# Optimization experiments

Measured on AMD Instinct MI355X. Metric: run time of the kernel, lower is better.

## Reference

```python
import jax, jax.numpy as jnp
import numpy as np

N, E, F_IN, F_E, HID, HEADS = 20000, 320000, 256, 32, 128, 4
NEG_SLOPE = 0.2  # PyG GATConv default negative_slope


def _segment_softmax(logits, seg, num_segments):
    # logits: [E, H] softmax over edges sharing the same destination node
    m = jax.ops.segment_max(logits, seg, num_segments=num_segments)
    m = jnp.where(jnp.isfinite(m), m, 0.0)
    e = jnp.exp(logits - m[seg])
    s = jax.ops.segment_sum(e, seg, num_segments=num_segments)
    return e / s[seg]


def _gat_layer(x, edge_attr, src, dst, W, We, a_src, a_dst, a_edge, bias, num_nodes):
    H, C = a_src.shape
    h = (x @ W).reshape(-1, H, C)            # [N, H, C]
    he = (edge_attr @ We).reshape(-1, H, C)  # [E, H, C]
    alpha = (h * a_src).sum(-1)[src] + (h * a_dst).sum(-1)[dst] + (he * a_edge).sum(-1)
    alpha = jax.nn.leaky_relu(alpha, NEG_SLOPE)          # [E, H]
    alpha = _segment_softmax(alpha, dst, num_nodes)
    out = jax.ops.segment_sum(h[src] * alpha[..., None], dst, num_segments=num_nodes)
    return out.reshape(num_nodes, H * C) + bias


def setup_inputs() -> dict:
    key = jax.random.key(0)
    ks = jax.random.split(key, 20)
    s1 = 1.0 / np.sqrt(F_IN)
    s2 = 1.0 / np.sqrt(HID * HEADS)
    se = 1.0 / np.sqrt(F_E)
    sh = 1.0 / np.sqrt(HID)
    return {
        "x": jax.random.normal(ks[0], (N, F_IN), jnp.float32),
        "edge_index": jax.random.randint(ks[1], (2, E), 0, N),
        "edge_attr": jax.random.normal(ks[2], (E, F_E), jnp.float32),
        # GAT layer 1: in=F_IN, heads=HEADS, out=HID, concat=True
        "W1": jax.random.normal(ks[3], (F_IN, HEADS * HID), jnp.float32) * s1,
        "We1": jax.random.normal(ks[4], (F_E, HEADS * HID), jnp.float32) * se,
        "as1": jax.random.normal(ks[5], (HEADS, HID), jnp.float32) * sh,
        "ad1": jax.random.normal(ks[6], (HEADS, HID), jnp.float32) * sh,
        "ae1": jax.random.normal(ks[7], (HEADS, HID), jnp.float32) * sh,
        "b1": jnp.zeros((HEADS * HID,), jnp.float32),
        # GAT layer 2: in=HEADS*HID, heads=1, out=HID
        "W2": jax.random.normal(ks[8], (HEADS * HID, HID), jnp.float32) * s2,
        "We2": jax.random.normal(ks[9], (F_E, HID), jnp.float32) * se,
        "as2": jax.random.normal(ks[10], (1, HID), jnp.float32) * sh,
        "ad2": jax.random.normal(ks[11], (1, HID), jnp.float32) * sh,
        "ae2": jax.random.normal(ks[12], (1, HID), jnp.float32) * sh,
        "b2": jnp.zeros((HID,), jnp.float32),
        # projection head: Linear(HID,HID) -> PReLU -> Linear(HID,HID)
        "P1": jax.random.normal(ks[13], (HID, HID), jnp.float32) * sh,
        "pb1": jnp.zeros((HID,), jnp.float32),
        "prelu_a": jnp.float32(0.25),
        "P2": jax.random.normal(ks[14], (HID, HID), jnp.float32) * sh,
        "pb2": jnp.zeros((HID,), jnp.float32),
    }


def reference(x, edge_index, edge_attr, W1, We1, as1, ad1, ae1, b1,
              W2, We2, as2, ad2, ae2, b2, P1, pb1, prelu_a, P2, pb2):
    # eval mode: edge dropout / feature dropout are no-ops
    ei = jnp.concatenate([edge_index, edge_index[::-1]], axis=1)  # add reversed edges
    ea = jnp.concatenate([edge_attr, edge_attr], axis=0)
    src, dst = ei[0], ei[1]
    n = x.shape[0]
    h = jax.nn.elu(_gat_layer(x, ea, src, dst, W1, We1, as1, ad1, ae1, b1, n))
    h = jax.nn.elu(_gat_layer(h, ea, src, dst, W2, We2, as2, ad2, ae2, b2, n))
    z = h @ P1 + pb1
    z = jnp.where(z > 0, z, prelu_a * z)  # PReLU (single shared parameter)
    h_proj = z @ P2 + pb2
    g = jax.nn.sigmoid(h_proj.mean(axis=0))
    return h_proj, g
```

## Files before the change

### kernel.cpp

```cpp
#include <hip/hip_runtime.h>
#include <hip/hip_bf16.h>


#define NN    20000
#define EE    320000
#define E2    640000
#define FIN   256
#define FE    32
#define HIDD  128
#define NHEAD 4
#define HH    512

typedef unsigned short ushort_t;
typedef short frag8 __attribute__((ext_vector_type(8)));
typedef float f32x4 __attribute__((ext_vector_type(4)));

__device__ inline ushort_t f2bf(float f){
  unsigned x = __float_as_uint(f);
  unsigned r = (x + 0x7fffu + ((x>>16)&1u)) >> 16;
  return (ushort_t)r;
}
__device__ inline float bf2f(ushort_t u){ return __uint_as_float(((unsigned)u)<<16); }
__device__ inline float lo_of(unsigned v){ return __uint_as_float(v<<16); }
__device__ inline float hi_of(unsigned v){ return __uint_as_float(v & 0xffff0000u); }

__global__ void prep(const int* __restrict__ ei, int* __restrict__ cnt,
                     const float* __restrict__ x, ushort_t* __restrict__ xb,
                     const float* __restrict__ W1, ushort_t* __restrict__ W1t,
                     const float* __restrict__ W2, ushort_t* __restrict__ W2t,
                     const float* __restrict__ P1, ushort_t* __restrict__ P1th, ushort_t* __restrict__ P1tl,
                     const float* __restrict__ P2, ushort_t* __restrict__ P2th, ushort_t* __restrict__ P2tl,
                     const float* __restrict__ We1, const float* __restrict__ ae1,
                     const float* __restrict__ We2, const float* __restrict__ ae2,
                     float* __restrict__ v1, float* __restrict__ v2){
  int b = blockIdx.x, tid = threadIdx.x;
  if(b < 2500){
    int e = b*256 + tid;
    int dst = (e < EE) ? ei[EE + e] : ei[e - EE];
    atomicAdd(&cnt[dst], 1);
  } else if(b < 7500){
    int i = (b-2500)*256 + tid;
    float4 v = ((const float4*)x)[i];
    ushort4 o; o.x=f2bf(v.x); o.y=f2bf(v.y); o.z=f2bf(v.z); o.w=f2bf(v.w);
    ((ushort4*)xb)[i] = o;
  } else if(b < 8012){
    int idx = (b-7500)*256 + tid;
    int k = idx>>9, n = idx&511;
    W1t[n*FIN + k] = f2bf(W1[idx]);
  } else if(b < 8268){
    int idx = (b-8012)*256 + tid;
    int k = idx>>7, n = idx&127;
    W2t[n*HH + k] = f2bf(W2[idx]);
  } else if(b < 8332){
    int idx = (b-8268)*256 + tid;
    int k = idx>>7, n = idx&127;
    float v = P1[idx];
    ushort_t h = f2bf(v);
    P1th[n*HIDD + k] = h;
    P1tl[n*HIDD + k] = f2bf(v - bf2f(h));
  } else if(b < 8396){
    int idx = (b-8332)*256 + tid;
    int k = idx>>7, n = idx&127;
    float v = P2[idx];
    ushort_t h = f2bf(v);
    P2th[n*HIDD + k] = h;
    P2tl[n*HIDD + k] = f2bf(v - bf2f(h));
  } else {
    if(tid < FE*NHEAD){
      int f = tid>>2, h = tid&3;
      float s = 0.f;
      for(int c=0;c<HIDD;c++) s += We1[f*HH + h*HIDD + c] * ae1[h*HIDD + c];
      v1[f*4+h] = s;
    } else if(tid < FE*NHEAD + FE){
      int f = tid - FE*NHEAD;
      float s = 0.f;
      for(int c=0;c<HIDD;c++) s += We2[f*HIDD + c] * ae2[c];
      v2[f] = s;
    }
  }
}

__global__ void scan_k(const int* __restrict__ cnt, int* __restrict__ rowptr){
  __shared__ int sums[1024];
  int tid = threadIdx.x;
  const int per = (NN + 1023)/1024;
  int base = tid*per;
  int s = 0;
  for(int i=0;i<per;i++){ int idx=base+i; if(idx<NN) s += cnt[idx]; }
  sums[tid] = s; __syncthreads();
  for(int off=1; off<1024; off<<=1){
    int v = (tid>=off)? sums[tid-off] : 0;
    __syncthreads();
    sums[tid] += v;
    __syncthreads();
  }
  int run = (tid==0)? 0 : sums[tid-1];
  for(int i=0;i<per;i++){
    int idx = base+i;
    if(idx<=NN) rowptr[idx] = run;
    if(idx<NN)  run += cnt[idx];
  }
}

__global__ void csr_fill(const int* __restrict__ ei, const float* __restrict__ ea,
                         const float* __restrict__ v1, const float* __restrict__ v2,
                         const int* __restrict__ rowptr, int* __restrict__ fcnt,
                         int* __restrict__ csrc, float* __restrict__ cae1, float* __restrict__ cae2){
  __shared__ float sv1[FE*NHEAD];
  __shared__ float sv2[FE];
  int tid = threadIdx.x;
  if(tid < FE*NHEAD) sv1[tid] = v1[tid];
  if(tid < FE)       sv2[tid] = v2[tid];
  __syncthreads();
  int e = blockIdx.x*256 + tid;
  int a = ei[e], b = ei[EE+e];
  const float4* er4 = (const float4*)(ea + (long)e*FE);
  float a0=0,a1=0,a2=0,a3=0,ab=0;
  #pragma unroll
  for(int f4=0; f4<FE/4; f4++){
    float4 t = er4[f4];
    float tv[4] = {t.x, t.y, t.z, t.w};
    #pragma unroll
    for(int c=0;c<4;c++){
      int f = f4*4+c;
      float t1 = tv[c];
      a0 += t1*sv1[f*4+0]; a1 += t1*sv1[f*4+1]; a2 += t1*sv1[f*4+2]; a3 += t1*sv1[f*4+3];
      ab += t1*sv2[f];
    }
  }
  float4 c4; c4.x=a0; c4.y=a1; c4.z=a2; c4.w=a3;
  int pos = rowptr[b] + atomicAdd(&fcnt[b], 1);
  csrc[pos] = a;
  *(float4*)(cae1 + (size_t)pos*4) = c4;
  cae2[pos] = ab;
  pos = rowptr[a] + atomicAdd(&fcnt[a], 1);
  csrc[pos] = b;
  *(float4*)(cae1 + (size_t)pos*4) = c4;
  cae2[pos] = ab;
}

__global__ __launch_bounds__(256) void gemm1_attn(const ushort_t* __restrict__ A, const ushort_t* __restrict__ Bt,
                                                  ushort_t* __restrict__ C, int M,
                                                  const float* __restrict__ as1, const float* __restrict__ ad1,
                                                  float* __restrict__ s1n, float* __restrict__ d1n){
  __shared__ ushort_t As[128*32];
  __shared__ ushort_t Bs[128*32];
  __shared__ float sred[2][128], dred[2][128];
  int tid = threadIdx.x;
  int head = blockIdx.x;
  int m0 = blockIdx.y*128, n0 = head*128;
  int w = tid>>6, lane = tid&63;
  int qr = (w>>1)*64, qc = (w&1)*64;
  int lrow = lane&15, koff = (lane>>4)*8;
  f32x4 acc[4][4] = {};
  for(int k0=0; k0<FIN; k0+=32){
    #pragma unroll
    for(int rep=0;rep<2;rep++){
      int segid = tid + rep*256;
      int row = segid>>2, off = (segid&3)*8;
      int gr = m0 + row;
      int4 va = (gr<M) ? *(const int4*)(A + (long)gr*FIN + k0 + off) : int4{0,0,0,0};
      *(int4*)&As[row*32 + off] = va;
      int4 vb = *(const int4*)(Bt + (long)(n0+row)*FIN + k0 + off);
      *(int4*)&Bs[row*32 + off] = vb;
    }
    __syncthreads();
    frag8 af[4], bfr[4];
    #pragma unroll
    for(int i=0;i<4;i++) af[i]  = *(const frag8*)&As[(qr + i*16 + lrow)*32 + koff];
    #pragma unroll
    for(int j=0;j<4;j++) bfr[j] = *(const frag8*)&Bs[(qc + j*16 + lrow)*32 + koff];
    #pragma unroll
    for(int i=0;i<4;i++)
      #pragma unroll
      for(int j=0;j<4;j++)
        acc[i][j] = __builtin_amdgcn_mfma_f32_16x16x32_bf16(af[i], bfr[j], acc[i][j], 0,0,0);
    __syncthreads();
  }
  #pragma unroll
  for(int i=0;i<4;i++)
    #pragma unroll
    for(int j=0;j<4;j++)
      #pragma unroll
      for(int r=0;r<4;r++){
        int row = m0 + qr + i*16 + (lane>>4)*4 + r;
        int col = n0 + qc + j*16 + (lane&15);
        if(row<M) C[(long)row*HH + col] = f2bf(acc[i][j][r]);
      }
  float a_s[4], a_d[4];
  #pragma unroll
  for(int j=0;j<4;j++){
    a_s[j] = as1[head*HIDD + qc + j*16 + (lane&15)];
    a_d[j] = ad1[head*HIDD + qc + j*16 + (lane&15)];
  }
  #pragma unroll
  for(int i=0;i<4;i++)
    #pragma unroll
    for(int r=0;r<4;r++){
      float sp = acc[i][0][r]*a_s[0] + acc[i][1][r]*a_s[1] + acc[i][2][r]*a_s[2] + acc[i][3][r]*a_s[3];
      float dp = acc[i][0][r]*a_d[0] + acc[i][1][r]*a_d[1] + acc[i][2][r]*a_d[2] + acc[i][3][r]*a_d[3];
      #pragma unroll
      for(int o=1;o<=8;o<<=1){ sp += __shfl_xor(sp,o,64); dp += __shfl_xor(dp,o,64); }
      if((lane&15)==0){
        int rl = qr + i*16 + (lane>>4)*4 + r;
        sred[w&1][rl] = sp;
        dred[w&1][rl] = dp;
      }
    }
  __syncthreads();
  if(tid < 128){
    int gr = m0 + tid;
    if(gr < M){
      s1n[gr*4 + head] = sred[0][tid] + sred[1][tid];
      d1n[gr*4 + head] = dred[0][tid] + dred[1][tid];
    }
  }
}

__global__ __launch_bounds__(256) void gemm64_attn(const ushort_t* __restrict__ A, const ushort_t* __restrict__ Bt,
                                                   ushort_t* __restrict__ C, int M,
                                                   const float* __restrict__ as2, const float* __restrict__ ad2,
                                                   float* __restrict__ s2n, float* __restrict__ d2n){
  __shared__ ushort_t As[64*32];
  __shared__ ushort_t Bs[128*32];
  __shared__ float sred[4][64], dred[4][64];
  int tid = threadIdx.x;
  int m0 = blockIdx.y*64;
  int w = tid>>6, lane = tid&63;
  int qc = w*32;
  int lrow = lane&15, koff = (lane>>4)*8;
  f32x4 acc[4][2] = {};
  for(int k0=0; k0<HH; k0+=32){
    {
      int row = tid>>2, off = (tid&3)*8;
      int gr = m0 + row;
      int4 va = (gr<M) ? *(const int4*)(A + (long)gr*HH + k0 + off) : int4{0,0,0,0};
      *(int4*)&As[row*32 + off] = va;
    }
    #pragma unroll
    for(int rep=0;rep<2;rep++){
      int segid = tid + rep*256;
      int row = segid>>2, off = (segid&3)*8;
      int4 vb = *(const int4*)(Bt + (long)row*HH + k0 + off);
      *(int4*)&Bs[row*32 + off] = vb;
    }
    __syncthreads();
    frag8 af[4], bfr[2];
    #pragma unroll
    for(int i=0;i<4;i++) af[i]  = *(const frag8*)&As[(i*16 + lrow)*32 + koff];
    #pragma unroll
    for(int j=0;j<2;j++) bfr[j] = *(const frag8*)&Bs[(qc + j*16 + lrow)*32 + koff];
    #pragma unroll
    for(int i=0;i<4;i++)
      #pragma unroll
      for(int j=0;j<2;j++)
        acc[i][j] = __builtin_amdgcn_mfma_f32_16x16x32_bf16(af[i], bfr[j], acc[i][j], 0,0,0);
    __syncthreads();
  }
  #pragma unroll
  for(int i=0;i<4;i++)
    #pragma unroll
    for(int j=0;j<2;j++)
      #pragma unroll
      for(int r=0;r<4;r++){
        int row = m0 + i*16 + (lane>>4)*4 + r;
        int col = qc + j*16 + (lane&15);
        if(row<M) C[(long)row*HIDD + col] = f2bf(acc[i][j][r]);
      }
  float a_s[2], a_d[2];
  #pragma unroll
  for(int j=0;j<2;j++){
    a_s[j] = as2[qc + j*16 + (lane&15)];
    a_d[j] = ad2[qc + j*16 + (lane&15)];
  }
  #pragma unroll
  for(int i=0;i<4;i++)
    #pragma unroll
    for(int r=0;r<4;r++){
      float sp = acc[i][0][r]*a_s[0] + acc[i][1][r]*a_s[1];
      float dp = acc[i][0][r]*a_d[0] + acc[i][1][r]*a_d[1];
      #pragma unroll
      for(int o=1;o<=8;o<<=1){ sp += __shfl_xor(sp,o,64); dp += __shfl_xor(dp,o,64); }
      if((lane&15)==0){
        int rl = i*16 + (lane>>4)*4 + r;
        sred[w][rl] = sp;
        dred[w][rl] = dp;
      }
    }
  __syncthreads();
  if(tid < 64){
    int gr = m0 + tid;
    if(gr < M){
      s2n[gr] = sred[0][tid]+sred[1][tid]+sred[2][tid]+sred[3][tid];
      d2n[gr] = dred[0][tid]+dred[1][tid]+dred[2][tid]+dred[3][tid];
    }
  }
}

__global__ __launch_bounds__(256) void mfma_proj(const float* __restrict__ A,
                                                 const ushort_t* __restrict__ Bth, const ushort_t* __restrict__ Btl,
                                                 float* __restrict__ C, int M,
                                                 const float* __restrict__ bias,
                                                 const float* __restrict__ prelu_a, int epi,
                                                 float* __restrict__ gbuf){
  __shared__ ushort_t Ash[64*32], Asl[64*32];
  __shared__ ushort_t Bsh[128*32], Bsl[128*32];
  int tid = threadIdx.x;
  int m0 = blockIdx.x*64;
  int w = tid>>6, lane = tid&63;
  int qc = w*32;
  int lrow = lane&15, koff2 = (lane>>4)*8;
  f32x4 acc[4][2] = {};
  for(int k0=0; k0<128; k0+=32){
    {
      int row = tid>>2, koff = (tid&3)*8;
      int gr = m0 + row;
      float4 u0{0,0,0,0}, u1{0,0,0,0};
      if(gr<M){
        u0 = *(const float4*)(A + (long)gr*HIDD + k0 + koff);
        u1 = *(const float4*)(A + (long)gr*HIDD + k0 + koff + 4);
      }
      float vv[8] = {u0.x,u0.y,u0.z,u0.w,u1.x,u1.y,u1.z,u1.w};
      unsigned ph[4], pl[4];
      #pragma unroll
      for(int c=0;c<4;c++){
        ushort_t h0 = f2bf(vv[2*c]),   l0 = f2bf(vv[2*c]   - bf2f(h0));
        ushort_t h1 = f2bf(vv[2*c+1]), l1 = f2bf(vv[2*c+1] - bf2f(h1));
        ph[c] = (unsigned)h0 | ((unsigned)h1<<16);
        pl[c] = (unsigned)l0 | ((unsigned)l1<<16);
      }
      *(uint4*)&Ash[row*32 + koff] = *(uint4*)ph;
      *(uint4*)&Asl[row*32 + koff] = *(uint4*)pl;
    }
    #pragma unroll
    for(int rep=0;rep<2;rep++){
      int segid = tid + rep*256;
      int row = segid>>2, off = (segid&3)*8;
      *(int4*)&Bsh[row*32 + off] = *(const int4*)(Bth + (long)row*HIDD + k0 + off);
      *(int4*)&Bsl[row*32 + off] = *(const int4*)(Btl + (long)row*HIDD + k0 + off);
    }
    __syncthreads();
    frag8 afh[4], afl[4], bfh[2], bfl[2];
    #pragma unroll
    for(int i=0;i<4;i++){
      afh[i] = *(const frag8*)&Ash[(i*16 + lrow)*32 + koff2];
      afl[i] = *(const frag8*)&Asl[(i*16 + lrow)*32 + koff2];
    }
    #pragma unroll
    for(int j=0;j<2;j++){
      bfh[j] = *(const frag8*)&Bsh[(qc + j*16 + lrow)*32 + koff2];
      bfl[j] = *(const frag8*)&Bsl[(qc + j*16 + lrow)*32 + koff2];
    }
    #pragma unroll
    for(int i=0;i<4;i++)
      #pragma unroll
      for(int j=0;j<2;j++){
        acc[i][j] = __builtin_amdgcn_mfma_f32_16x16x32_bf16(afh[i], bfh[j], acc[i][j], 0,0,0);
        acc[i][j] = __builtin_amdgcn_mfma_f32_16x16x32_bf16(afh[i], bfl[j], acc[i][j], 0,0,0);
        acc[i][j] = __builtin_amdgcn_mfma_f32_16x16x32_bf16(afl[i], bfh[j], acc[i][j], 0,0,0);
      }
    __syncthreads();
  }
  float ap = (epi==1)? prelu_a[0] : 0.f;
  #pragma unroll
  for(int i=0;i<4;i++)
    #pragma unroll
    for(int j=0;j<2;j++)
      #pragma unroll
      for(int r=0;r<4;r++){
        int row = m0 + i*16 + (lane>>4)*4 + r;
        int col = qc + j*16 + (lane&15);
        if(row<M){
          float v = acc[i][j][r] + bias[col];
          if(epi==1) v = v>0.f? v : ap*v;
          acc[i][j][r] = v;
          C[(long)row*HIDD + col] = v;
        } else acc[i][j][r] = 0.f;
      }
  if(epi==0){
    #pragma unroll
    for(int j=0;j<2;j++){
      float cp = 0.f;
      #pragma unroll
      for(int i=0;i<4;i++)
        #pragma unroll
        for(int r=0;r<4;r++) cp += acc[i][j][r];
      cp += __shfl_xor(cp,16,64);
      cp += __shfl_xor(cp,32,64);
      if((lane>>4)==0) atomicAdd(&gbuf[qc + j*16 + (lane&15)], cp);
    }
  }
}


__global__ __launch_bounds__(512) void agg1(const ushort_t* __restrict__ h1b, const int* __restrict__ rowptr,
                     const int* __restrict__ csrc,
                     const float* __restrict__ s1n, const float* __restrict__ d1n,
                     const float* __restrict__ cae1, float* __restrict__ elog,
                     const float* __restrict__ b1, ushort_t* __restrict__ out1b){
  __shared__ float part[4][512];
  int tid = threadIdx.x;
  int nodeLoc = tid>>7;
  int wv = (tid>>6)&1;
  int lane = tid&63;
  int n = blockIdx.x*4 + nodeLoc;
  int beg = rowptr[n], end = rowptr[n+1];
  int h12 = lane&3;
  float dh = d1n[n*4 + h12];
  float m = -1e30f, ss = 0.f;
  for(int base=beg; base<end; base+=16){
    int e = base + (lane>>2);
    if(e<end){
      float t = s1n[csrc[e]*4 + h12] + dh + cae1[e*4 + h12];
      t = t>0.f? t : 0.2f*t;
      if(wv==0) elog[e*4 + h12] = t;
      float nm = fmaxf(m, t);
      ss = ss*__expf(m-nm) + __expf(t-nm);
      m = nm;
    }
  }
  #pragma unroll
  for(int o=4;o<=32;o<<=1){
    float mo = __shfl_xor(m, o, 64), so = __shfl_xor(ss, o, 64);
    float nm = fmaxf(m, mo);
    ss = ss*__expf(m-nm) + so*__expf(mo-nm);
    m = nm;
  }
  float inv = ss>0.f ? 1.f/ss : 0.f;
  int hq = lane>>4;
  float mq   = __shfl(m,   hq, 64);
  float invq = __shfl(inv, hq, 64);
  __syncthreads();
  int deg = end-beg;
  int half = (deg+1)>>1;
  int gb = beg + wv*half;
  int ge = wv ? end : beg+half;
  float acc[8] = {};
  int i = gb;
  for(; i+3<ge; i+=4){
    int s0 = csrc[i], s1 = csrc[i+1], s2 = csrc[i+2], s3 = csrc[i+3];
    float w0 = __expf(elog[i*4 + hq]     - mq)*invq;
    float w1 = __expf(elog[(i+1)*4 + hq] - mq)*invq;
    float w2 = __expf(elog[(i+2)*4 + hq] - mq)*invq;
    float w3 = __expf(elog[(i+3)*4 + hq] - mq)*invq;
    uint4 v0 = *(const uint4*)(h1b + (long)s0*HH + lane*8);
    uint4 v1 = *(const uint4*)(h1b + (long)s1*HH + lane*8);
    uint4 v2 = *(const uint4*)(h1b + (long)s2*HH + lane*8);
    uint4 v3 = *(const uint4*)(h1b + (long)s3*HH + lane*8);
    acc[0] += w0*lo_of(v0.x) + w1*lo_of(v1.x) + w2*lo_of(v2.x) + w3*lo_of(v3.x);
    acc[1] += w0*hi_of(v0.x) + w1*hi_of(v1.x) + w2*hi_of(v2.x) + w3*hi_of(v3.x);
    acc[2] += w0*lo_of(v0.y) + w1*lo_of(v1.y) + w2*lo_of(v2.y) + w3*lo_of(v3.y);
    acc[3] += w0*hi_of(v0.y) + w1*hi_of(v1.y) + w2*hi_of(v2.y) + w3*hi_of(v3.y);
    acc[4] += w0*lo_of(v0.z) + w1*lo_of(v1.z) + w2*lo_of(v2.z) + w3*lo_of(v3.z);
    acc[5] += w0*hi_of(v0.z) + w1*hi_of(v1.z) + w2*hi_of(v2.z) + w3*hi_of(v3.z);
    acc[6] += w0*lo_of(v0.w) + w1*lo_of(v1.w) + w2*lo_of(v2.w) + w3*lo_of(v3.w);
    acc[7] += w0*hi_of(v0.w) + w1*hi_of(v1.w) + w2*hi_of(v2.w) + w3*hi_of(v3.w);
  }
  for(; i<ge; i++){
    int s0 = csrc[i];
    float w0 = __expf(elog[i*4 + hq] - mq)*invq;
    uint4 v0 = *(const uint4*)(h1b + (long)s0*HH + lane*8);
    acc[0] += w0*lo_of(v0.x); acc[1] += w0*hi_of(v0.x);
    acc[2] += w0*lo_of(v0.y); acc[3] += w0*hi_of(v0.y);
    acc[4] += w0*lo_of(v0.z); acc[5] += w0*hi_of(v0.z);
    acc[6] += w0*lo_of(v0.w); acc[7] += w0*hi_of(v0.w);
  }
  if(wv==1){
    #pragma unroll
    for(int c=0;c<8;c++) part[nodeLoc][c*64 + lane] = acc[c];
  }
  __syncthreads();
  if(wv==0){
    #pragma unroll
    for(int c=0;c<8;c++) acc[c] += part[nodeLoc][c*64 + lane];
    float4 bl = ((const float4*)b1)[lane*2];
    float4 bh = ((const float4*)b1)[lane*2+1];
    float bb[8] = {bl.x,bl.y,bl.z,bl.w,bh.x,bh.y,bh.z,bh.w};
    ushort_t o8[8];
    #pragma unroll
    for(int c=0;c<8;c++){
      float o = acc[c] + bb[c];
      o8[c] = f2bf(o>0.f? o : __expf(o)-1.f);
    }
    uint4 pk;
    pk.x = (unsigned)o8[0] | ((unsigned)o8[1]<<16);
    pk.y = (unsigned)o8[2] | ((unsigned)o8[3]<<16);
    pk.z = (unsigned)o8[4] | ((unsigned)o8[5]<<16);
    pk.w = (unsigned)o8[6] | ((unsigned)o8[7]<<16);
    *(uint4*)(out1b + (long)n*HH + lane*8) = pk;
  }
}

__global__ void agg2(const ushort_t* __restrict__ h2b, const int* __restrict__ rowptr,
                     const int* __restrict__ csrc,
                     const float* __restrict__ s2n, const float* __restrict__ d2n,
                     const float* __restrict__ cae2, float* __restrict__ elog,
                     const float* __restrict__ b2, float* __restrict__ out2){
  int n = blockIdx.x*4 + (threadIdx.x>>6);
  int lane = threadIdx.x&63;
  int beg = rowptr[n], end = rowptr[n+1];
  float dn = d2n[n];
  float m = -1e30f, ss = 0.f;
  for(int e=beg+lane; e<end; e+=64){
    float t = s2n[csrc[e]] + dn + cae2[e];
    t = t>0.f? t : 0.2f*t;
    elog[e] = t;
    float nm = fmaxf(m, t);
    ss = ss*__expf(m-nm) + __expf(t-nm);
    m = nm;
  }
  #pragma unroll
  for(int o=1;o<=32;o<<=1){
    float mo = __shfl_xor(m, o, 64), so = __shfl_xor(ss, o, 64);
    float nm = fmaxf(m, mo);
    ss = ss*__expf(m-nm) + so*__expf(mo-nm);
    m = nm;
  }
  float inv = ss>0.f ? 1.f/ss : 0.f;
  float a0=0.f, a1=0.f;
  int i = beg;
  for(; i+3<end; i+=4){
    int s0 = csrc[i], s1 = csrc[i+1], s2 = csrc[i+2], s3 = csrc[i+3];
    float w0 = __expf(elog[i]-m)*inv;
    float w1 = __expf(elog[i+1]-m)*inv;
    float w2 = __expf(elog[i+2]-m)*inv;
    float w3 = __expf(elog[i+3]-m)*inv;
    unsigned v0 = *(const unsigned*)(h2b + (long)s0*HIDD + 2*lane);
    unsigned v1 = *(const unsigned*)(h2b + (long)s1*HIDD + 2*lane);
    unsigned v2 = *(const unsigned*)(h2b + (long)s2*HIDD + 2*lane);
    unsigned v3 = *(const unsigned*)(h2b + (long)s3*HIDD + 2*lane);
    a0 += w0*lo_of(v0) + w1*lo_of(v1) + w2*lo_of(v2) + w3*lo_of(v3);
    a1 += w0*hi_of(v0) + w1*hi_of(v1) + w2*hi_of(v2) + w3*hi_of(v3);
  }
  for(; i<end; i++){
    float w0 = __expf(elog[i]-m)*inv;
    unsigned v0 = *(const unsigned*)(h2b + (long)csrc[i]*HIDD + 2*lane);
    a0 += w0*lo_of(v0); a1 += w0*hi_of(v0);
  }
  float o0 = a0 + b2[2*lane];
  float o1 = a1 + b2[2*lane+1];
  float2 pk;
  pk.x = o0>0.f? o0 : __expf(o0)-1.f;
  pk.y = o1>0.f? o1 : __expf(o1)-1.f;
  *(float2*)(out2 + (long)n*HIDD + 2*lane) = pk;
}

__global__ void sigmoid_g(const float* __restrict__ gbuf, float* __restrict__ gout){
  int c = threadIdx.x;
  float m = gbuf[c] * (1.0f/NN);
  gout[c] = 1.f/(1.f+__expf(-m));
}


extern "C" void kernel_launch(void* const* d_in, const int* in_sizes, int n_in,
                              void* d_out, int out_size, void* d_ws, size_t ws_size,
                              hipStream_t stream){
  const float* x    = (const float*)d_in[0];
  const int*   ei   = (const int*)  d_in[1];
  const float* ea   = (const float*)d_in[2];
  const float* W1   = (const float*)d_in[3];
  const float* We1  = (const float*)d_in[4];
  const float* as1  = (const float*)d_in[5];
  const float* ad1  = (const float*)d_in[6];
  const float* ae1  = (const float*)d_in[7];
  const float* b1   = (const float*)d_in[8];
  const float* W2   = (const float*)d_in[9];
  const float* We2  = (const float*)d_in[10];
  const float* as2  = (const float*)d_in[11];
  const float* ad2  = (const float*)d_in[12];
  const float* ae2  = (const float*)d_in[13];
  const float* b2   = (const float*)d_in[14];
  const float* P1   = (const float*)d_in[15];
  const float* pb1  = (const float*)d_in[16];
  const float* pra  = (const float*)d_in[17];
  const float* P2   = (const float*)d_in[18];
  const float* pb2  = (const float*)d_in[19];
  float* out = (float*)d_out;

  char* wsp = (char*)d_ws;
  size_t off = 0;
  auto alloc = [&](size_t bytes)->char*{
    char* p = wsp + off;
    off += (bytes + 255) & ~(size_t)255;
    return p;
  };
  ushort_t* h1b  = (ushort_t*)alloc(sizeof(ushort_t)*(size_t)NN*HH);
  ushort_t* out1b= (ushort_t*)alloc(sizeof(ushort_t)*(size_t)NN*HH);
  ushort_t* h2b  = (ushort_t*)alloc(sizeof(ushort_t)*(size_t)NN*HIDD);
  float*    out2 = (float*)  alloc(sizeof(float)*(size_t)NN*HIDD);
  float*    zb   = (float*)  alloc(sizeof(float)*(size_t)NN*HIDD);
  ushort_t* xb   = (ushort_t*)alloc(sizeof(ushort_t)*(size_t)NN*FIN);
  ushort_t* W1t  = (ushort_t*)alloc(sizeof(ushort_t)*(size_t)HH*FIN);
  ushort_t* W2t  = (ushort_t*)alloc(sizeof(ushort_t)*(size_t)HIDD*HH);
  ushort_t* P1th = (ushort_t*)alloc(sizeof(ushort_t)*(size_t)HIDD*HIDD);
  ushort_t* P1tl = (ushort_t*)alloc(sizeof(ushort_t)*(size_t)HIDD*HIDD);
  ushort_t* P2th = (ushort_t*)alloc(sizeof(ushort_t)*(size_t)HIDD*HIDD);
  ushort_t* P2tl = (ushort_t*)alloc(sizeof(ushort_t)*(size_t)HIDD*HIDD);
  float* s1n   = (float*)alloc(sizeof(float)*NN*NHEAD);
  float* d1n   = (float*)alloc(sizeof(float)*NN*NHEAD);
  float* s2n   = (float*)alloc(sizeof(float)*NN);
  float* d2n   = (float*)alloc(sizeof(float)*NN);
  float* v1    = (float*)alloc(sizeof(float)*FE*NHEAD);
  float* v2    = (float*)alloc(sizeof(float)*FE);
  float* cae1  = (float*)alloc(sizeof(float)*(size_t)E2*NHEAD);
  float* elog1 = (float*)alloc(sizeof(float)*(size_t)E2*NHEAD);
  float* cae2  = (float*)alloc(sizeof(float)*(size_t)E2);
  float* elog2 = (float*)alloc(sizeof(float)*(size_t)E2);
  int*   rowptr= (int*)  alloc(sizeof(int)*(NN+1));
  int*   csrc  = (int*)  alloc(sizeof(int)*(size_t)E2);
  int*   cnt   = (int*)  alloc(sizeof(int)*NN);
  int*   fcnt  = (int*)  alloc(sizeof(int)*NN);
  float* gbuf  = (float*)alloc(sizeof(float)*HIDD);

  hipMemsetAsync(cnt, 0, 80128 + 80128 + 512, stream);

  prep    <<<8397, 256, 0, stream>>>(ei, cnt, x, xb, W1, W1t, W2, W2t,
                                     P1, P1th, P1tl, P2, P2th, P2tl,
                                     We1, ae1, We2, ae2, v1, v2);
  scan_k  <<<1, 1024, 0, stream>>>(cnt, rowptr);
  csr_fill<<<EE/256, 256, 0, stream>>>(ei, ea, v1, v2, rowptr, fcnt, csrc, cae1, cae2);

  gemm1_attn<<<dim3(NHEAD, (NN+127)/128), 256, 0, stream>>>(xb, W1t, h1b, NN, as1, ad1, s1n, d1n);
  agg1      <<<NN/4, 512, 0, stream>>>(h1b, rowptr, csrc, s1n, d1n, cae1, elog1, b1, out1b);

  gemm64_attn<<<dim3(1, (NN+63)/64), 256, 0, stream>>>(out1b, W2t, h2b, NN, as2, ad2, s2n, d2n);
  agg2       <<<NN/4, 256, 0, stream>>>(h2b, rowptr, csrc, s2n, d2n, cae2, elog2, b2, out2);

  mfma_proj<<<(NN+63)/64, 256, 0, stream>>>(out2, P1th, P1tl, zb, NN, pb1, pra, 1, nullptr);
  mfma_proj<<<(NN+63)/64, 256, 0, stream>>>(zb,  P2th, P2tl, out, NN, pb2, nullptr, 0, gbuf);

  sigmoid_g<<<1, 128, 0, stream>>>(gbuf, out + (size_t)NN*HIDD);
}
```

Baseline: 432.7 us.

## Fuse CSR fill with GEMM1, cache logits in LDS, fuse projection GEMMs

The CSR fill and the first attention GEMM now run in one launch, with the first 1250 blocks doing edge work and the rest doing GEMM tiles, so the two independent stages can overlap. Both aggregation kernels keep per-edge logits and source indices in LDS (up to CAP edges per node) and no longer write or read global elog buffers. agg1 now uses one wave per node instead of two waves splitting each node's edges. The two projection GEMMs are merged into one kernel that keeps the PReLU intermediate in LDS, which drops the zb round trip through global memory. The costs are larger LDS footprint, a recompute path for nodes above CAP, and less parallelism per node in agg1.

```diff
diff --git a/kernel.cpp b/kernel.cpp
--- a/kernel.cpp
+++ b/kernel.cpp
@@ -10,6 +10,8 @@
 #define HIDD  128
 #define NHEAD 4
 #define HH    512
+#define CAP   160
+#define AW    132
 
 typedef unsigned short ushort_t;
 typedef short frag8 __attribute__((ext_vector_type(8)));
@@ -102,53 +104,56 @@
   }
 }
 
-__global__ void csr_fill(const int* __restrict__ ei, const float* __restrict__ ea,
-                         const float* __restrict__ v1, const float* __restrict__ v2,
-                         const int* __restrict__ rowptr, int* __restrict__ fcnt,
-                         int* __restrict__ csrc, float* __restrict__ cae1, float* __restrict__ cae2){
+__global__ __launch_bounds__(256) void csr_gemm1(
+    const int* __restrict__ ei, const float* __restrict__ ea,
+    const float* __restrict__ v1, const float* __restrict__ v2,
+    const int* __restrict__ rowptr, int* __restrict__ fcnt,
+    int* __restrict__ csrc, float* __restrict__ cae1, float* __restrict__ cae2,
+    const ushort_t* __restrict__ A, const ushort_t* __restrict__ Bt,
+    ushort_t* __restrict__ C, int M,
+    const float* __restrict__ as1, const float* __restrict__ ad1,
+    float* __restrict__ s1n, float* __restrict__ d1n){
+  __shared__ ushort_t As[128*32];
+  __shared__ ushort_t Bs[128*32];
+  __shared__ float sred[2][128], dred[2][128];
   __shared__ float sv1[FE*NHEAD];
   __shared__ float sv2[FE];
   int tid = threadIdx.x;
-  if(tid < FE*NHEAD) sv1[tid] = v1[tid];
-  if(tid < FE)       sv2[tid] = v2[tid];
-  __syncthreads();
-  int e = blockIdx.x*256 + tid;
-  int a = ei[e], b = ei[EE+e];
-  const float4* er4 = (const float4*)(ea + (long)e*FE);
-  float a0=0,a1=0,a2=0,a3=0,ab=0;
-  #pragma unroll
-  for(int f4=0; f4<FE/4; f4++){
-    float4 t = er4[f4];
-    float tv[4] = {t.x, t.y, t.z, t.w};
-    #pragma unroll
-    for(int c=0;c<4;c++){
-      int f = f4*4+c;
-      float t1 = tv[c];
-      a0 += t1*sv1[f*4+0]; a1 += t1*sv1[f*4+1]; a2 += t1*sv1[f*4+2]; a3 += t1*sv1[f*4+3];
-      ab += t1*sv2[f];
-    }
-  }
-  float4 c4; c4.x=a0; c4.y=a1; c4.z=a2; c4.w=a3;
-  int pos = rowptr[b] + atomicAdd(&fcnt[b], 1);
-  csrc[pos] = a;
-  *(float4*)(cae1 + (size_t)pos*4) = c4;
-  cae2[pos] = ab;
-  pos = rowptr[a] + atomicAdd(&fcnt[a], 1);
-  csrc[pos] = b;
-  *(float4*)(cae1 + (size_t)pos*4) = c4;
-  cae2[pos] = ab;
-}
-
-__global__ __launch_bounds__(256) void gemm1_attn(const ushort_t* __restrict__ A, const ushort_t* __restrict__ Bt,
-                                                  ushort_t* __restrict__ C, int M,
-                                                  const float* __restrict__ as1, const float* __restrict__ ad1,
-                                                  float* __restrict__ s1n, float* __restrict__ d1n){
-  __shared__ ushort_t As[128*32];
-  __shared__ ushort_t Bs[128*32];
-  __shared__ float sred[2][128], dred[2][128];
-  int tid = threadIdx.x;
-  int head = blockIdx.x;
-  int m0 = blockIdx.y*128, n0 = head*128;
+  int b = blockIdx.x;
+  if(b < 1250){
+    if(tid < FE*NHEAD) sv1[tid] = v1[tid];
+    if(tid < FE)       sv2[tid] = v2[tid];
+    __syncthreads();
+    int e = b*256 + tid;
+    int a = ei[e], bb = ei[EE+e];
+    const float4* er4 = (const float4*)(ea + (long)e*FE);
+    float a0=0,a1=0,a2=0,a3=0,ab=0;
+    #pragma unroll
+    for(int f4=0; f4<FE/4; f4++){
+      float4 t = er4[f4];
+      float tv[4] = {t.x, t.y, t.z, t.w};
+      #pragma unroll
+      for(int c=0;c<4;c++){
+        int f = f4*4+c;
+        float t1 = tv[c];
+        a0 += t1*sv1[f*4+0]; a1 += t1*sv1[f*4+1]; a2 += t1*sv1[f*4+2]; a3 += t1*sv1[f*4+3];
+        ab += t1*sv2[f];
+      }
+    }
+    float4 c4; c4.x=a0; c4.y=a1; c4.z=a2; c4.w=a3;
+    int pos = rowptr[bb] + atomicAdd(&fcnt[bb], 1);
+    csrc[pos] = a;
+    *(float4*)(cae1 + (size_t)pos*4) = c4;
+    cae2[pos] = ab;
+    pos = rowptr[a] + atomicAdd(&fcnt[a], 1);
+    csrc[pos] = bb;
+    *(float4*)(cae1 + (size_t)pos*4) = c4;
+    cae2[pos] = ab;
+    return;
+  }
+  int g = b - 1250;
+  int head = g & 3;
+  int m0 = (g>>2)*128, n0 = head*128;
   int w = tid>>6, lane = tid&63;
   int qr = (w>>1)*64, qc = (w&1)*64;
   int lrow = lane&15, koff = (lane>>4)*8;
@@ -297,123 +302,32 @@
   }
 }
 
-__global__ __launch_bounds__(256) void mfma_proj(const float* __restrict__ A,
-                                                 const ushort_t* __restrict__ Bth, const ushort_t* __restrict__ Btl,
-                                                 float* __restrict__ C, int M,
-                                                 const float* __restrict__ bias,
-                                                 const float* __restrict__ prelu_a, int epi,
-                                                 float* __restrict__ gbuf){
-  __shared__ ushort_t Ash[64*32], Asl[64*32];
-  __shared__ ushort_t Bsh[128*32], Bsl[128*32];
-  int tid = threadIdx.x;
-  int m0 = blockIdx.x*64;
-  int w = tid>>6, lane = tid&63;
-  int qc = w*32;
-  int lrow = lane&15, koff2 = (lane>>4)*8;
-  f32x4 acc[4][2] = {};
-  for(int k0=0; k0<128; k0+=32){
-    {
-      int row = tid>>2, koff = (tid&3)*8;
-      int gr = m0 + row;
-      float4 u0{0,0,0,0}, u1{0,0,0,0};
-      if(gr<M){
-        u0 = *(const float4*)(A + (long)gr*HIDD + k0 + koff);
-        u1 = *(const float4*)(A + (long)gr*HIDD + k0 + koff + 4);
-      }
-      float vv[8] = {u0.x,u0.y,u0.z,u0.w,u1.x,u1.y,u1.z,u1.w};
-      unsigned ph[4], pl[4];
-      #pragma unroll
-      for(int c=0;c<4;c++){
-        ushort_t h0 = f2bf(vv[2*c]),   l0 = f2bf(vv[2*c]   - bf2f(h0));
-        ushort_t h1 = f2bf(vv[2*c+1]), l1 = f2bf(vv[2*c+1] - bf2f(h1));
-        ph[c] = (unsigned)h0 | ((unsigned)h1<<16);
-        pl[c] = (unsigned)l0 | ((unsigned)l1<<16);
-      }
-      *(uint4*)&Ash[row*32 + koff] = *(uint4*)ph;
-      *(uint4*)&Asl[row*32 + koff] = *(uint4*)pl;
-    }
-    #pragma unroll
-    for(int rep=0;rep<2;rep++){
-      int segid = tid + rep*256;
-      int row = segid>>2, off = (segid&3)*8;
-      *(int4*)&Bsh[row*32 + off] = *(const int4*)(Bth + (long)row*HIDD + k0 + off);
-      *(int4*)&Bsl[row*32 + off] = *(const int4*)(Btl + (long)row*HIDD + k0 + off);
-    }
-    __syncthreads();
-    frag8 afh[4], afl[4], bfh[2], bfl[2];
-    #pragma unroll
-    for(int i=0;i<4;i++){
-      afh[i] = *(const frag8*)&Ash[(i*16 + lrow)*32 + koff2];
-      afl[i] = *(const frag8*)&Asl[(i*16 + lrow)*32 + koff2];
-    }
-    #pragma unroll
-    for(int j=0;j<2;j++){
-      bfh[j] = *(const frag8*)&Bsh[(qc + j*16 + lrow)*32 + koff2];
-      bfl[j] = *(const frag8*)&Bsl[(qc + j*16 + lrow)*32 + koff2];
-    }
-    #pragma unroll
-    for(int i=0;i<4;i++)
-      #pragma unroll
-      for(int j=0;j<2;j++){
-        acc[i][j] = __builtin_amdgcn_mfma_f32_16x16x32_bf16(afh[i], bfh[j], acc[i][j], 0,0,0);
-        acc[i][j] = __builtin_amdgcn_mfma_f32_16x16x32_bf16(afh[i], bfl[j], acc[i][j], 0,0,0);
-        acc[i][j] = __builtin_amdgcn_mfma_f32_16x16x32_bf16(afl[i], bfh[j], acc[i][j], 0,0,0);
-      }
-    __syncthreads();
-  }
-  float ap = (epi==1)? prelu_a[0] : 0.f;
-  #pragma unroll
-  for(int i=0;i<4;i++)
-    #pragma unroll
-    for(int j=0;j<2;j++)
-      #pragma unroll
-      for(int r=0;r<4;r++){
-        int row = m0 + i*16 + (lane>>4)*4 + r;
-        int col = qc + j*16 + (lane&15);
-        if(row<M){
-          float v = acc[i][j][r] + bias[col];
-          if(epi==1) v = v>0.f? v : ap*v;
-          acc[i][j][r] = v;
-          C[(long)row*HIDD + col] = v;
-        } else acc[i][j][r] = 0.f;
-      }
-  if(epi==0){
-    #pragma unroll
-    for(int j=0;j<2;j++){
-      float cp = 0.f;
-      #pragma unroll
-      for(int i=0;i<4;i++)
-        #pragma unroll
-        for(int r=0;r<4;r++) cp += acc[i][j][r];
-      cp += __shfl_xor(cp,16,64);
-      cp += __shfl_xor(cp,32,64);
-      if((lane>>4)==0) atomicAdd(&gbuf[qc + j*16 + (lane&15)], cp);
-    }
-  }
-}
-
-
-__global__ __launch_bounds__(512) void agg1(const ushort_t* __restrict__ h1b, const int* __restrict__ rowptr,
+__global__ __launch_bounds__(256) void agg1(const ushort_t* __restrict__ h1b, const int* __restrict__ rowptr,
                      const int* __restrict__ csrc,
                      const float* __restrict__ s1n, const float* __restrict__ d1n,
-                     const float* __restrict__ cae1, float* __restrict__ elog,
+                     const float* __restrict__ cae1,
                      const float* __restrict__ b1, ushort_t* __restrict__ out1b){
-  __shared__ float part[4][512];
+  __shared__ float stlog[4][CAP*4];
+  __shared__ int   sidx[4][CAP];
   int tid = threadIdx.x;
-  int nodeLoc = tid>>7;
-  int wv = (tid>>6)&1;
-  int lane = tid&63;
-  int n = blockIdx.x*4 + nodeLoc;
+  int wv = tid>>6, lane = tid&63;
+  int n = blockIdx.x*4 + wv;
   int beg = rowptr[n], end = rowptr[n+1];
+  int deg = end - beg;
   int h12 = lane&3;
   float dh = d1n[n*4 + h12];
   float m = -1e30f, ss = 0.f;
   for(int base=beg; base<end; base+=16){
     int e = base + (lane>>2);
     if(e<end){
-      float t = s1n[csrc[e]*4 + h12] + dh + cae1[e*4 + h12];
+      int s = csrc[e];
+      float t = s1n[s*4 + h12] + dh + cae1[e*4 + h12];
       t = t>0.f? t : 0.2f*t;
-      if(wv==0) elog[e*4 + h12] = t;
+      int j = e - beg;
+      if(j < CAP){
+        stlog[wv][j*4 + h12] = t;
+        if(h12==0) sidx[wv][j] = s;
+      }
       float nm = fmaxf(m, t);
       ss = ss*__expf(m-nm) + __expf(t-nm);
       m = nm;
@@ -430,19 +344,16 @@
   int hq = lane>>4;
   float mq   = __shfl(m,   hq, 64);
   float invq = __shfl(inv, hq, 64);
-  __syncthreads();
-  int deg = end-beg;
-  int half = (deg+1)>>1;
-  int gb = beg + wv*half;
-  int ge = wv ? end : beg+half;
+  float dhq  = d1n[n*4 + hq];
+  int capn = deg < CAP ? deg : CAP;
   float acc[8] = {};
-  int i = gb;
-  for(; i+3<ge; i+=4){
-    int s0 = csrc[i], s1 = csrc[i+1], s2 = csrc[i+2], s3 = csrc[i+3];
-    float w0 = __expf(elog[i*4 + hq]     - mq)*invq;
-    float w1 = __expf(elog[(i+1)*4 + hq] - mq)*invq;
-    float w2 = __expf(elog[(i+2)*4 + hq] - mq)*invq;
-    float w3 = __expf(elog[(i+3)*4 + hq] - mq)*invq;
+  int j = 0;
+  for(; j+3<capn; j+=4){
+    int s0 = sidx[wv][j], s1 = sidx[wv][j+1], s2 = sidx[wv][j+2], s3 = sidx[wv][j+3];
+    float w0 = __expf(stlog[wv][(j  )*4 + hq] - mq)*invq;
+    float w1 = __expf(stlog[wv][(j+1)*4 + hq] - mq)*invq;
+    float w2 = __expf(stlog[wv][(j+2)*4 + hq] - mq)*invq;
+    float w3 = __expf(stlog[wv][(j+3)*4 + hq] - mq)*invq;
     uint4 v0 = *(const uint4*)(h1b + (long)s0*HH + lane*8);
     uint4 v1 = *(const uint4*)(h1b + (long)s1*HH + lane*8);
     uint4 v2 = *(const uint4*)(h1b + (long)s2*HH + lane*8);
@@ -456,55 +367,64 @@
     acc[6] += w0*lo_of(v0.w) + w1*lo_of(v1.w) + w2*lo_of(v2.w) + w3*lo_of(v3.w);
     acc[7] += w0*hi_of(v0.w) + w1*hi_of(v1.w) + w2*hi_of(v2.w) + w3*hi_of(v3.w);
   }
-  for(; i<ge; i++){
-    int s0 = csrc[i];
-    float w0 = __expf(elog[i*4 + hq] - mq)*invq;
+  for(; j<capn; j++){
+    int s0 = sidx[wv][j];
+    float w0 = __expf(stlog[wv][j*4 + hq] - mq)*invq;
     uint4 v0 = *(const uint4*)(h1b + (long)s0*HH + lane*8);
     acc[0] += w0*lo_of(v0.x); acc[1] += w0*hi_of(v0.x);
     acc[2] += w0*lo_of(v0.y); acc[3] += w0*hi_of(v0.y);
     acc[4] += w0*lo_of(v0.z); acc[5] += w0*hi_of(v0.z);
     acc[6] += w0*lo_of(v0.w); acc[7] += w0*hi_of(v0.w);
   }
-  if(wv==1){
-    #pragma unroll
-    for(int c=0;c<8;c++) part[nodeLoc][c*64 + lane] = acc[c];
-  }
-  __syncthreads();
-  if(wv==0){
-    #pragma unroll
-    for(int c=0;c<8;c++) acc[c] += part[nodeLoc][c*64 + lane];
-    float4 bl = ((const float4*)b1)[lane*2];
-    float4 bh = ((const float4*)b1)[lane*2+1];
-    float bb[8] = {bl.x,bl.y,bl.z,bl.w,bh.x,bh.y,bh.z,bh.w};
-    ushort_t o8[8];
-    #pragma unroll
-    for(int c=0;c<8;c++){
-      float o = acc[c] + bb[c];
-      o8[c] = f2bf(o>0.f? o : __expf(o)-1.f);
-    }
-    uint4 pk;
-    pk.x = (unsigned)o8[0] | ((unsigned)o8[1]<<16);
-    pk.y = (unsigned)o8[2] | ((unsigned)o8[3]<<16);
-    pk.z = (unsigned)o8[4] | ((unsigned)o8[5]<<16);
-    pk.w = (unsigned)o8[6] | ((unsigned)o8[7]<<16);
-    *(uint4*)(out1b + (long)n*HH + lane*8) = pk;
-  }
-}
-
-__global__ void agg2(const ushort_t* __restrict__ h2b, const int* __restrict__ rowptr,
+  for(; j<deg; j++){
+    int e = beg + j;
+    int s0 = csrc[e];
+    float t = s1n[s0*4 + hq] + dhq + cae1[e*4 + hq];
+    t = t>0.f? t : 0.2f*t;
+    float w0 = __expf(t - mq)*invq;
+    uint4 v0 = *(const uint4*)(h1b + (long)s0*HH + lane*8);
+    acc[0] += w0*lo_of(v0.x); acc[1] += w0*hi_of(v0.x);
+    acc[2] += w0*lo_of(v0.y); acc[3] += w0*hi_of(v0.y);
+    acc[4] += w0*lo_of(v0.z); acc[5] += w0*hi_of(v0.z);
+    acc[6] += w0*lo_of(v0.w); acc[7] += w0*hi_of(v0.w);
+  }
+  float4 bl = ((const float4*)b1)[lane*2];
+  float4 bh = ((const float4*)b1)[lane*2+1];
+  float bb[8] = {bl.x,bl.y,bl.z,bl.w,bh.x,bh.y,bh.z,bh.w};
+  ushort_t o8[8];
+  #pragma unroll
+  for(int c=0;c<8;c++){
+    float o = acc[c] + bb[c];
+    o8[c] = f2bf(o>0.f? o : __expf(o)-1.f);
+  }
+  uint4 pk;
+  pk.x = (unsigned)o8[0] | ((unsigned)o8[1]<<16);
+  pk.y = (unsigned)o8[2] | ((unsigned)o8[3]<<16);
+  pk.z = (unsigned)o8[4] | ((unsigned)o8[5]<<16);
+  pk.w = (unsigned)o8[6] | ((unsigned)o8[7]<<16);
+  *(uint4*)(out1b + (long)n*HH + lane*8) = pk;
+}
+
+__global__ __launch_bounds__(256) void agg2(const ushort_t* __restrict__ h2b, const int* __restrict__ rowptr,
                      const int* __restrict__ csrc,
                      const float* __restrict__ s2n, const float* __restrict__ d2n,
-                     const float* __restrict__ cae2, float* __restrict__ elog,
+                     const float* __restrict__ cae2,
                      const float* __restrict__ b2, float* __restrict__ out2){
-  int n = blockIdx.x*4 + (threadIdx.x>>6);
-  int lane = threadIdx.x&63;
+  __shared__ float stl[4][CAP];
+  __shared__ int   sid[4][CAP];
+  int tid = threadIdx.x;
+  int wv = tid>>6, lane = tid&63;
+  int n = blockIdx.x*4 + wv;
   int beg = rowptr[n], end = rowptr[n+1];
+  int deg = end - beg;
   float dn = d2n[n];
   float m = -1e30f, ss = 0.f;
   for(int e=beg+lane; e<end; e+=64){
-    float t = s2n[csrc[e]] + dn + cae2[e];
+    int s = csrc[e];
+    float t = s2n[s] + dn + cae2[e];
     t = t>0.f? t : 0.2f*t;
-    elog[e] = t;
+    int j = e - beg;
+    if(j < CAP){ stl[wv][j] = t; sid[wv][j] = s; }
     float nm = fmaxf(m, t);
     ss = ss*__expf(m-nm) + __expf(t-nm);
     m = nm;
@@ -517,14 +437,15 @@
     m = nm;
   }
   float inv = ss>0.f ? 1.f/ss : 0.f;
+  int capn = deg < CAP ? deg : CAP;
   float a0=0.f, a1=0.f;
-  int i = beg;
-  for(; i+3<end; i+=4){
-    int s0 = csrc[i], s1 = csrc[i+1], s2 = csrc[i+2], s3 = csrc[i+3];
-    float w0 = __expf(elog[i]-m)*inv;
-    float w1 = __expf(elog[i+1]-m)*inv;
-    float w2 = __expf(elog[i+2]-m)*inv;
-    float w3 = __expf(elog[i+3]-m)*inv;
+  int j = 0;
+  for(; j+3<capn; j+=4){
+    int s0 = sid[wv][j], s1 = sid[wv][j+1], s2 = sid[wv][j+2], s3 = sid[wv][j+3];
+    float w0 = __expf(stl[wv][j]  -m)*inv;
+    float w1 = __expf(stl[wv][j+1]-m)*inv;
+    float w2 = __expf(stl[wv][j+2]-m)*inv;
+    float w3 = __expf(stl[wv][j+3]-m)*inv;
     unsigned v0 = *(const unsigned*)(h2b + (long)s0*HIDD + 2*lane);
     unsigned v1 = *(const unsigned*)(h2b + (long)s1*HIDD + 2*lane);
     unsigned v2 = *(const unsigned*)(h2b + (long)s2*HIDD + 2*lane);
@@ -532,9 +453,18 @@
     a0 += w0*lo_of(v0) + w1*lo_of(v1) + w2*lo_of(v2) + w3*lo_of(v3);
     a1 += w0*hi_of(v0) + w1*hi_of(v1) + w2*hi_of(v2) + w3*hi_of(v3);
   }
-  for(; i<end; i++){
-    float w0 = __expf(elog[i]-m)*inv;
-    unsigned v0 = *(const unsigned*)(h2b + (long)csrc[i]*HIDD + 2*lane);
+  for(; j<capn; j++){
+    float w0 = __expf(stl[wv][j]-m)*inv;
+    unsigned v0 = *(const unsigned*)(h2b + (long)sid[wv][j]*HIDD + 2*lane);
+    a0 += w0*lo_of(v0); a1 += w0*hi_of(v0);
+  }
+  for(; j<deg; j++){
+    int e = beg + j;
+    int s0 = csrc[e];
+    float t = s2n[s0] + dn + cae2[e];
+    t = t>0.f? t : 0.2f*t;
+    float w0 = __expf(t-m)*inv;
+    unsigned v0 = *(const unsigned*)(h2b + (long)s0*HIDD + 2*lane);
     a0 += w0*lo_of(v0); a1 += w0*hi_of(v0);
   }
   float o0 = a0 + b2[2*lane];
@@ -543,6 +473,143 @@
   pk.x = o0>0.f? o0 : __expf(o0)-1.f;
   pk.y = o1>0.f? o1 : __expf(o1)-1.f;
   *(float2*)(out2 + (long)n*HIDD + 2*lane) = pk;
+}
+
+__global__ __launch_bounds__(256) void proj_fused(const float* __restrict__ A,
+    const ushort_t* __restrict__ P1th, const ushort_t* __restrict__ P1tl,
+    const ushort_t* __restrict__ P2th, const ushort_t* __restrict__ P2tl,
+    const float* __restrict__ pb1, const float* __restrict__ pra,
+    const float* __restrict__ pb2, float* __restrict__ OUT, int M,
+    float* __restrict__ gbuf){
+  __shared__ ushort_t Ah[64*AW], Al[64*AW];
+  __shared__ ushort_t Bh[128*32], Bl[128*32];
+  int tid = threadIdx.x;
+  int m0 = blockIdx.x*64;
+  int w = tid>>6, lane = tid&63;
+  int qc = w*32;
+  int lrow = lane&15, koff2 = (lane>>4)*8;
+  f32x4 acc[4][2] = {};
+  {
+    int row = tid>>2, cb = (tid&3)*8;
+    int gr = m0 + row;
+    for(int c0=0;c0<HIDD;c0+=32){
+      float4 u0{0,0,0,0}, u1{0,0,0,0};
+      if(gr<M){
+        u0 = *(const float4*)(A + (long)gr*HIDD + c0 + cb);
+        u1 = *(const float4*)(A + (long)gr*HIDD + c0 + cb + 4);
+      }
+      float vv[8] = {u0.x,u0.y,u0.z,u0.w,u1.x,u1.y,u1.z,u1.w};
+      unsigned ph[4], pl[4];
+      #pragma unroll
+      for(int c=0;c<4;c++){
+        ushort_t h0 = f2bf(vv[2*c]),   l0 = f2bf(vv[2*c]   - bf2f(h0));
+        ushort_t h1 = f2bf(vv[2*c+1]), l1 = f2bf(vv[2*c+1] - bf2f(h1));
+        ph[c] = (unsigned)h0 | ((unsigned)h1<<16);
+        pl[c] = (unsigned)l0 | ((unsigned)l1<<16);
+      }
+      *(uint4*)&Ah[row*AW + c0 + cb] = *(uint4*)ph;
+      *(uint4*)&Al[row*AW + c0 + cb] = *(uint4*)pl;
+    }
+  }
+  __syncthreads();
+  for(int k0=0;k0<HIDD;k0+=32){
+    #pragma unroll
+    for(int rep=0;rep<2;rep++){
+      int segid = tid + rep*256;
+      int row = segid>>2, off = (segid&3)*8;
+      *(int4*)&Bh[row*32 + off] = *(const int4*)(P1th + (long)row*HIDD + k0 + off);
+      *(int4*)&Bl[row*32 + off] = *(const int4*)(P1tl + (long)row*HIDD + k0 + off);
+    }
+    __syncthreads();
+    frag8 afh[4], afl[4], bfh[2], bfl[2];
+    #pragma unroll
+    for(int i=0;i<4;i++){
+      afh[i] = *(const frag8*)&Ah[(i*16 + lrow)*AW + k0 + koff2];
+      afl[i] = *(const frag8*)&Al[(i*16 + lrow)*AW + k0 + koff2];
+    }
+    #pragma unroll
+    for(int j=0;j<2;j++){
+      bfh[j] = *(const frag8*)&Bh[(qc + j*16 + lrow)*32 + koff2];
+      bfl[j] = *(const frag8*)&Bl[(qc + j*16 + lrow)*32 + koff2];
+    }
+    #pragma unroll
+    for(int i=0;i<4;i++)
+      #pragma unroll
+      for(int j=0;j<2;j++){
+        acc[i][j] = __builtin_amdgcn_mfma_f32_16x16x32_bf16(afh[i], bfh[j], acc[i][j], 0,0,0);
+        acc[i][j] = __builtin_amdgcn_mfma_f32_16x16x32_bf16(afh[i], bfl[j], acc[i][j], 0,0,0);
+        acc[i][j] = __builtin_amdgcn_mfma_f32_16x16x32_bf16(afl[i], bfh[j], acc[i][j], 0,0,0);
+      }
+    __syncthreads();
+  }
+  float ap = pra[0];
+  #pragma unroll
+  for(int i=0;i<4;i++)
+    #pragma unroll
+    for(int j=0;j<2;j++)
+      #pragma unroll
+      for(int r=0;r<4;r++){
+        int row = i*16 + (lane>>4)*4 + r;
+        int col = qc + j*16 + (lane&15);
+        float v = acc[i][j][r] + pb1[col];
+        v = v>0.f? v : ap*v;
+        ushort_t h = f2bf(v);
+        Ah[row*AW + col] = h;
+        Al[row*AW + col] = f2bf(v - bf2f(h));
+        acc[i][j][r] = 0.f;
+      }
+  __syncthreads();
+  for(int k0=0;k0<HIDD;k0+=32){
+    #pragma unroll
+    for(int rep=0;rep<2;rep++){
+      int segid = tid + rep*256;
+      int row = segid>>2, off = (segid&3)*8;
+      *(int4*)&Bh[row*32 + off] = *(const int4*)(P2th + (long)row*HIDD + k0 + off);
+      *(int4*)&Bl[row*32 + off] = *(const int4*)(P2tl + (long)row*HIDD + k0 + off);
+    }
+    __syncthreads();
+    frag8 afh[4], afl[4], bfh[2], bfl[2];
+    #pragma unroll
+    for(int i=0;i<4;i++){
+      afh[i] = *(const frag8*)&Ah[(i*16 + lrow)*AW + k0 + koff2];
+      afl[i] = *(const frag8*)&Al[(i*16 + lrow)*AW + k0 + koff2];
+    }
+    #pragma unroll
+    for(int j=0;j<2;j++){
+      bfh[j] = *(const frag8*)&Bh[(qc + j*16 + lrow)*32 + koff2];
+      bfl[j] = *(const frag8*)&Bl[(qc + j*16 + lrow)*32 + koff2];
+    }
+    #pragma unroll
+    for(int i=0;i<4;i++)
+      #pragma unroll
+      for(int j=0;j<2;j++){
+        acc[i][j] = __builtin_amdgcn_mfma_f32_16x16x32_bf16(afh[i], bfh[j], acc[i][j], 0,0,0);
+        acc[i][j] = __builtin_amdgcn_mfma_f32_16x16x32_bf16(afh[i], bfl[j], acc[i][j], 0,0,0);
+        acc[i][j] = __builtin_amdgcn_mfma_f32_16x16x32_bf16(afl[i], bfh[j], acc[i][j], 0,0,0);
+      }
+    __syncthreads();
+  }
+  float cs[2] = {0.f, 0.f};
+  #pragma unroll
+  for(int i=0;i<4;i++)
+    #pragma unroll
+    for(int j=0;j<2;j++)
+      #pragma unroll
+      for(int r=0;r<4;r++){
+        int rowg = m0 + i*16 + (lane>>4)*4 + r;
+        int col = qc + j*16 + (lane&15);
+        if(rowg<M){
+          float v = acc[i][j][r] + pb2[col];
+          OUT[(long)rowg*HIDD + col] = v;
+          cs[j] += v;
+        }
+      }
+  #pragma unroll
+  for(int j=0;j<2;j++){
+    cs[j] += __shfl_xor(cs[j],16,64);
+    cs[j] += __shfl_xor(cs[j],32,64);
+    if((lane>>4)==0) atomicAdd(&gbuf[qc + j*16 + (lane&15)], cs[j]);
+  }
 }
 
 __global__ void sigmoid_g(const float* __restrict__ gbuf, float* __restrict__ gout){
@@ -588,7 +655,6 @@
   ushort_t* out1b= (ushort_t*)alloc(sizeof(ushort_t)*(size_t)NN*HH);
   ushort_t* h2b  = (ushort_t*)alloc(sizeof(ushort_t)*(size_t)NN*HIDD);
   float*    out2 = (float*)  alloc(sizeof(float)*(size_t)NN*HIDD);
-  float*    zb   = (float*)  alloc(sizeof(float)*(size_t)NN*HIDD);
   ushort_t* xb   = (ushort_t*)alloc(sizeof(ushort_t)*(size_t)NN*FIN);
   ushort_t* W1t  = (ushort_t*)alloc(sizeof(ushort_t)*(size_t)HH*FIN);
   ushort_t* W2t  = (ushort_t*)alloc(sizeof(ushort_t)*(size_t)HIDD*HH);
@@ -603,9 +669,7 @@
   float* v1    = (float*)alloc(sizeof(float)*FE*NHEAD);
   float* v2    = (float*)alloc(sizeof(float)*FE);
   float* cae1  = (float*)alloc(sizeof(float)*(size_t)E2*NHEAD);
-  float* elog1 = (float*)alloc(sizeof(float)*(size_t)E2*NHEAD);
   float* cae2  = (float*)alloc(sizeof(float)*(size_t)E2);
-  float* elog2 = (float*)alloc(sizeof(float)*(size_t)E2);
   int*   rowptr= (int*)  alloc(sizeof(int)*(NN+1));
   int*   csrc  = (int*)  alloc(sizeof(int)*(size_t)E2);
   int*   cnt   = (int*)  alloc(sizeof(int)*NN);
@@ -614,20 +678,16 @@
 
   hipMemsetAsync(cnt, 0, 80128 + 80128 + 512, stream);
 
-  prep    <<<8397, 256, 0, stream>>>(ei, cnt, x, xb, W1, W1t, W2, W2t,
-                                     P1, P1th, P1tl, P2, P2th, P2tl,
-                                     We1, ae1, We2, ae2, v1, v2);
-  scan_k  <<<1, 1024, 0, stream>>>(cnt, rowptr);
-  csr_fill<<<EE/256, 256, 0, stream>>>(ei, ea, v1, v2, rowptr, fcnt, csrc, cae1, cae2);
-
-  gemm1_attn<<<dim3(NHEAD, (NN+127)/128), 256, 0, stream>>>(xb, W1t, h1b, NN, as1, ad1, s1n, d1n);
-  agg1      <<<NN/4, 512, 0, stream>>>(h1b, rowptr, csrc, s1n, d1n, cae1, elog1, b1, out1b);
-
+  prep     <<<8397, 256, 0, stream>>>(ei, cnt, x, xb, W1, W1t, W2, W2t,
+                                      P1, P1th, P1tl, P2, P2th, P2tl,
+                                      We1, ae1, We2, ae2, v1, v2);
+  scan_k   <<<1, 1024, 0, stream>>>(cnt, rowptr);
+  csr_gemm1<<<1250 + 628, 256, 0, stream>>>(ei, ea, v1, v2, rowptr, fcnt, csrc, cae1, cae2,
+                                            xb, W1t, h1b, NN, as1, ad1, s1n, d1n);
+  agg1     <<<NN/4, 256, 0, stream>>>(h1b, rowptr, csrc, s1n, d1n, cae1, b1, out1b);
   gemm64_attn<<<dim3(1, (NN+63)/64), 256, 0, stream>>>(out1b, W2t, h2b, NN, as2, ad2, s2n, d2n);
-  agg2       <<<NN/4, 256, 0, stream>>>(h2b, rowptr, csrc, s2n, d2n, cae2, elog2, b2, out2);
-
-  mfma_proj<<<(NN+63)/64, 256, 0, stream>>>(out2, P1th, P1tl, zb, NN, pb1, pra, 1, nullptr);
-  mfma_proj<<<(NN+63)/64, 256, 0, stream>>>(zb,  P2th, P2tl, out, NN, pb2, nullptr, 0, gbuf);
-
+  agg2     <<<NN/4, 256, 0, stream>>>(h2b, rowptr, csrc, s2n, d2n, cae2, b2, out2);
+  proj_fused<<<(NN+63)/64, 256, 0, stream>>>(out2, P1th, P1tl, P2th, P2tl,
+                                             pb1, pra, pb2, out, NN, gbuf);
   sigmoid_g<<<1, 128, 0, stream>>>(gbuf, out + (size_t)NN*HIDD);
 }
```

New measurement: 394.8 us. 8.8% less time.
